# Performance work log

Hardware: AMD Instinct MI355X
Metric: run time of the kernel (lower is better)

The kernel has to match this reference:

```python
import jax, jax.numpy as jnp
import numpy as np


def _gather_corner(flat_feats, iz, iy, ix, H, W, B, F, Hg, Wg):
    # flat_feats: [B, F, D*H*W]; iz/iy/ix: [B, Hg, Wg] int32 (already clamped)
    lin = (iz * H + iy) * W + ix                      # [B, Hg, Wg]
    lin = jnp.broadcast_to(lin.reshape(B, 1, Hg * Wg), (B, F, Hg * Wg))
    return jnp.take_along_axis(flat_feats, lin, axis=2).reshape(B, F, Hg, Wg)


def setup_inputs() -> dict:
    key = jax.random.key(0)
    k1, k2 = jax.random.split(key)
    input_feats = jax.random.normal(k1, (4, 8, 128, 128, 128), dtype=jnp.float32)
    sampling_grid = jax.random.normal(k2, (4, 512, 512, 3), dtype=jnp.float32)
    return {"input_feats": input_feats, "sampling_grid": sampling_grid}


def reference(input_feats, sampling_grid):
    B, F, D, H, W = input_feats.shape
    Hg, Wg = sampling_grid.shape[1], sampling_grid.shape[2]

    # map grid from [-1,1] to voxel coordinates [0, dim-1]
    g = jnp.clip(sampling_grid, -1.0, 1.0)
    scale = jnp.array([W - 1.0, H - 1.0, D - 1.0], dtype=sampling_grid.dtype)
    g = (g + 1.0) * 0.5 * scale                      # [B, Hg, Wg, 3] in x,y,z order
    x, y, z = g[..., 0], g[..., 1], g[..., 2]

    x0 = jnp.floor(x); y0 = jnp.floor(y); z0 = jnp.floor(z)
    u = (x - x0)[:, None]                            # [B,1,Hg,Wg]
    v = (y - y0)[:, None]
    w = (z - z0)[:, None]

    # nearest grid_sample with align_corners=True on integer coords == clamped index
    def clampi(a, hi):
        return jnp.clip(a, 0, hi).astype(jnp.int32)

    ix0 = clampi(x0, W - 1); ix1 = clampi(x0 + 1.0, W - 1)
    iy0 = clampi(y0, H - 1); iy1 = clampi(y0 + 1.0, H - 1)
    iz0 = clampi(z0, D - 1); iz1 = clampi(z0 + 1.0, D - 1)

    flat = input_feats.reshape(B, F, D * H * W)
    gc = lambda iz, iy, ix: _gather_corner(flat, iz, iy, ix, H, W, B, F, Hg, Wg)

    c000 = gc(iz0, iy0, ix0); c001 = gc(iz1, iy0, ix0)
    c010 = gc(iz0, iy1, ix0); c011 = gc(iz1, iy1, ix0)
    c100 = gc(iz0, iy0, ix1); c101 = gc(iz1, iy0, ix1)
    c110 = gc(iz0, iy1, ix1); c111 = gc(iz1, iy1, ix1)

    out = ((1 - u) * (1 - v) * (1 - w) * c000 + (1 - u) * (1 - v) * w * c001
           + (1 - u) * v * (1 - w) * c010 + (1 - u) * v * w * c011
           + u * (1 - v) * (1 - w) * c100 + u * (1 - v) * w * c101
           + u * v * (1 - w) * c110 + u * v * w * c111)
    return out  # [B, F, Hg, Wg]
```

## Files before the change

kernel.cpp:

```cpp
#include <hip/hip_runtime.h>
#include <hip/hip_fp16.h>


#define NB 4
#define NF 8
#define ND 128
#define NH 128
#define NW 128
#define HG 512
#define WG 512

__global__ __launch_bounds__(256) void transform_kernel(
    const float* __restrict__ feats, __half* __restrict__ T)
{
    const size_t S = (size_t)ND * NH * NW;
    size_t tid = (size_t)blockIdx.x * blockDim.x + threadIdx.x;
    size_t b  = tid / (S / 4);
    size_t s4 = (tid - b * (S / 4)) * 4;

    const float* fb = feats + b * NF * S;
    __half* tb = T + (b * S + s4) * NF;

    float4 vals[NF];
#pragma unroll
    for (int f = 0; f < NF; ++f)
        vals[f] = *(const float4*)(fb + (size_t)f * S + s4);

#pragma unroll
    for (int i = 0; i < 4; ++i) {
        alignas(16) __half2 hv[4];
#pragma unroll
        for (int f = 0; f < 4; ++f) {
            float a = ((const float*)&vals[2 * f])[i];
            float c = ((const float*)&vals[2 * f + 1])[i];
            hv[f] = __floats2half2_rn(a, c);
        }
        *(uint4*)(tb + (size_t)i * NF) = *(const uint4*)hv;
    }
}

__device__ __forceinline__ void row_accum(
    const __half* __restrict__ tb, size_t rowbase, bool hi,
    float wr, float um, float u, float acc[NF])
{
    uint4 lov = *(const uint4*)(tb + rowbase);
    uint4 hiv = *(const uint4*)(tb + rowbase + NF);
    uint4 c0 = hi ? hiv : lov;
    const uint4& c1 = hiv;

    const unsigned* p0 = (const unsigned*)&c0;
    const unsigned* p1 = (const unsigned*)&c1;
#pragma unroll
    for (int j = 0; j < 4; ++j) {
        unsigned u0 = p0[j], u1 = p1[j];
        float2 f0 = __half22float2(*(const __half2*)&u0);
        float2 f1 = __half22float2(*(const __half2*)&u1);
        acc[2 * j]     += wr * (um * f0.x + u * f1.x);
        acc[2 * j + 1] += wr * (um * f0.y + u * f1.y);
    }
}

__global__ __launch_bounds__(256) void trilerp_half_kernel(
    const __half* __restrict__ T,
    const float* __restrict__ grid,
    float* __restrict__ out)
{
    const int P = HG * WG;
    int idx = blockIdx.x * blockDim.x + threadIdx.x;
    int b = idx >> 18;
    int p = idx & (P - 1);

    const float* g = grid + (size_t)idx * 3;
    float x = g[0], y = g[1], z = g[2];

    x = fminf(fmaxf(x, -1.0f), 1.0f);
    y = fminf(fmaxf(y, -1.0f), 1.0f);
    z = fminf(fmaxf(z, -1.0f), 1.0f);
    x = (x + 1.0f) * 0.5f * (float)(NW - 1);
    y = (y + 1.0f) * 0.5f * (float)(NH - 1);
    z = (z + 1.0f) * 0.5f * (float)(ND - 1);

    float xf = floorf(x), yf = floorf(y), zf = floorf(z);
    float u = x - xf, v = y - yf, w = z - zf;
    float um = 1.0f - u, vm = 1.0f - v, wm = 1.0f - w;

    int ix0 = min(max((int)xf, 0), NW - 1);
    int iy0 = min(max((int)yf, 0), NH - 1);
    int iy1 = min(iy0 + 1, NH - 1);
    int iz0 = min(max((int)zf, 0), ND - 1);
    int iz1 = min(iz0 + 1, ND - 1);

    int xb = min(ix0, NW - 2);
    bool hi = (ix0 != xb);

    const __half* tb = T + (size_t)b * ((size_t)ND * NH * NW) * NF;
    size_t r00 = ((size_t)(iz0 * NH + iy0) * NW + xb) * NF;
    size_t r01 = ((size_t)(iz0 * NH + iy1) * NW + xb) * NF;
    size_t r10 = ((size_t)(iz1 * NH + iy0) * NW + xb) * NF;
    size_t r11 = ((size_t)(iz1 * NH + iy1) * NW + xb) * NF;

    float acc[NF];
#pragma unroll
    for (int f = 0; f < NF; ++f) acc[f] = 0.0f;

    row_accum(tb, r00, hi, wm * vm, um, u, acc);
    row_accum(tb, r01, hi, wm * v,  um, u, acc);
    row_accum(tb, r10, hi, w  * vm, um, u, acc);
    row_accum(tb, r11, hi, w  * v,  um, u, acc);

    float* o = out + (size_t)b * NF * P + p;
#pragma unroll
    for (int f = 0; f < NF; ++f)
        o[(size_t)f * P] = acc[f];
}

__global__ __launch_bounds__(256) void trilerp_f32_kernel(
    const float* __restrict__ feats,
    const float* __restrict__ grid,
    float* __restrict__ out)
{
    const int P = HG * WG;
    int idx = blockIdx.x * blockDim.x + threadIdx.x;
    int b = idx >> 18;
    int p = idx & (P - 1);

    const float* g = grid + (size_t)idx * 3;
    float x = g[0], y = g[1], z = g[2];
    x = fminf(fmaxf(x, -1.0f), 1.0f);
    y = fminf(fmaxf(y, -1.0f), 1.0f);
    z = fminf(fmaxf(z, -1.0f), 1.0f);
    x = (x + 1.0f) * 0.5f * (float)(NW - 1);
    y = (y + 1.0f) * 0.5f * (float)(NH - 1);
    z = (z + 1.0f) * 0.5f * (float)(ND - 1);

    float xf = floorf(x), yf = floorf(y), zf = floorf(z);
    float u = x - xf, v = y - yf, w = z - zf;

    int ix0 = min(max((int)xf, 0), NW - 1);
    int ix1 = min(ix0 + 1, NW - 1);
    int iy0 = min(max((int)yf, 0), NH - 1);
    int iy1 = min(iy0 + 1, NH - 1);
    int iz0 = min(max((int)zf, 0), ND - 1);
    int iz1 = min(iz0 + 1, ND - 1);

    float um = 1.0f - u, vm = 1.0f - v, wm = 1.0f - w;
    float w000 = um * vm * wm, w100 = u * vm * wm;
    float w010 = um * v * wm,  w110 = u * v * wm;
    float w001 = um * vm * w,  w101 = u * vm * w;
    float w011 = um * v * w,   w111 = u * v * w;

    int off00 = (iz0 * NH + iy0) * NW;
    int off01 = (iz0 * NH + iy1) * NW;
    int off10 = (iz1 * NH + iy0) * NW;
    int off11 = (iz1 * NH + iy1) * NW;

    const size_t fstride = (size_t)ND * NH * NW;
    const float* fb = feats + (size_t)b * NF * fstride;
    float* o = out + (size_t)b * NF * P + p;

#pragma unroll
    for (int f = 0; f < NF; ++f) {
        const float* fp = fb + (size_t)f * fstride;
        float r = w000 * fp[off00 + ix0] + w100 * fp[off00 + ix1]
                + w010 * fp[off01 + ix0] + w110 * fp[off01 + ix1]
                + w001 * fp[off10 + ix0] + w101 * fp[off10 + ix1]
                + w011 * fp[off11 + ix0] + w111 * fp[off11 + ix1];
        o[(size_t)f * P] = r;
    }
}

extern "C" void kernel_launch(void* const* d_in, const int* in_sizes, int n_in,
                              void* d_out, int out_size, void* d_ws, size_t ws_size,
                              hipStream_t stream) {
    const float* feats = (const float*)d_in[0];
    const float* grid  = (const float*)d_in[1];
    float* out = (float*)d_out;

    const size_t needed = (size_t)NB * ND * NH * NW * NF * sizeof(__half);

    if (ws_size >= needed) {
        __half* T = (__half*)d_ws;
        const int tthreads = NB * ND * NH * NW / 4;
        transform_kernel<<<tthreads / 256, 256, 0, stream>>>(feats, T);
        const int total = NB * HG * WG;
        trilerp_half_kernel<<<total / 256, 256, 0, stream>>>(T, grid, out);
    } else {
        const int total = NB * HG * WG;
        trilerp_f32_kernel<<<total / 256, 256, 0, stream>>>(feats, grid, out);
    }
}
```

Before: 446.2 us.

## Pipeline per-batch fp16 transform with gather of previous batch in one launch

Replaces the two full-size launches with a sequence of per-batch stage launches. Each launch splits its blocks between converting batch k to the fp16 channel-interleaved layout and gathering/interpolating batch k-1, so the bandwidth-bound transform overlaps with the latency-bound gather. It adds extra launches and grid-stride loops, and each half gets only 1024 blocks, which may leave one phase underutilized or imbalanced.

```diff
diff --git a/kernel.cpp b/kernel.cpp
--- a/kernel.cpp
+++ b/kernel.cpp
@@ -10,32 +10,36 @@
 #define HG 512
 #define WG 512
 
-__global__ __launch_bounds__(256) void transform_kernel(
-    const float* __restrict__ feats, __half* __restrict__ T)
-{
-    const size_t S = (size_t)ND * NH * NW;
-    size_t tid = (size_t)blockIdx.x * blockDim.x + threadIdx.x;
-    size_t b  = tid / (S / 4);
-    size_t s4 = (tid - b * (S / 4)) * 4;
-
-    const float* fb = feats + b * NF * S;
-    __half* tb = T + (b * S + s4) * NF;
-
-    float4 vals[NF];
-#pragma unroll
-    for (int f = 0; f < NF; ++f)
-        vals[f] = *(const float4*)(fb + (size_t)f * S + s4);
-
-#pragma unroll
-    for (int i = 0; i < 4; ++i) {
-        alignas(16) __half2 hv[4];
-#pragma unroll
-        for (int f = 0; f < 4; ++f) {
-            float a = ((const float*)&vals[2 * f])[i];
-            float c = ((const float*)&vals[2 * f + 1])[i];
-            hv[f] = __floats2half2_rn(a, c);
+#define SVOX ((size_t)ND * NH * NW)
+#define NPTS (HG * WG)
+
+__device__ __forceinline__ void do_transform(
+    const float* __restrict__ feats, __half* __restrict__ T,
+    int b, int tid, int nthreads)
+{
+    const float* fb = feats + (size_t)b * NF * SVOX;
+    const int nitems = (int)(SVOX / 4);
+
+    for (int it = tid; it < nitems; it += nthreads) {
+        size_t s4 = (size_t)it * 4;
+        __half* tb = T + ((size_t)b * SVOX + s4) * NF;
+
+        float4 vals[NF];
+#pragma unroll
+        for (int f = 0; f < NF; ++f)
+            vals[f] = *(const float4*)(fb + (size_t)f * SVOX + s4);
+
+#pragma unroll
+        for (int i = 0; i < 4; ++i) {
+            alignas(16) __half2 hv[4];
+#pragma unroll
+            for (int f = 0; f < 4; ++f) {
+                float a = ((const float*)&vals[2 * f])[i];
+                float c = ((const float*)&vals[2 * f + 1])[i];
+                hv[f] = __floats2half2_rn(a, c);
+            }
+            *(uint4*)(tb + (size_t)i * NF) = *(const uint4*)hv;
         }
-        *(uint4*)(tb + (size_t)i * NF) = *(const uint4*)hv;
     }
 }
 
@@ -60,58 +64,72 @@
     }
 }
 
-__global__ __launch_bounds__(256) void trilerp_half_kernel(
-    const __half* __restrict__ T,
-    const float* __restrict__ grid,
-    float* __restrict__ out)
-{
-    const int P = HG * WG;
-    int idx = blockIdx.x * blockDim.x + threadIdx.x;
-    int b = idx >> 18;
-    int p = idx & (P - 1);
-
-    const float* g = grid + (size_t)idx * 3;
-    float x = g[0], y = g[1], z = g[2];
-
-    x = fminf(fmaxf(x, -1.0f), 1.0f);
-    y = fminf(fmaxf(y, -1.0f), 1.0f);
-    z = fminf(fmaxf(z, -1.0f), 1.0f);
-    x = (x + 1.0f) * 0.5f * (float)(NW - 1);
-    y = (y + 1.0f) * 0.5f * (float)(NH - 1);
-    z = (z + 1.0f) * 0.5f * (float)(ND - 1);
-
-    float xf = floorf(x), yf = floorf(y), zf = floorf(z);
-    float u = x - xf, v = y - yf, w = z - zf;
-    float um = 1.0f - u, vm = 1.0f - v, wm = 1.0f - w;
-
-    int ix0 = min(max((int)xf, 0), NW - 1);
-    int iy0 = min(max((int)yf, 0), NH - 1);
-    int iy1 = min(iy0 + 1, NH - 1);
-    int iz0 = min(max((int)zf, 0), ND - 1);
-    int iz1 = min(iz0 + 1, ND - 1);
-
-    int xb = min(ix0, NW - 2);
-    bool hi = (ix0 != xb);
-
-    const __half* tb = T + (size_t)b * ((size_t)ND * NH * NW) * NF;
-    size_t r00 = ((size_t)(iz0 * NH + iy0) * NW + xb) * NF;
-    size_t r01 = ((size_t)(iz0 * NH + iy1) * NW + xb) * NF;
-    size_t r10 = ((size_t)(iz1 * NH + iy0) * NW + xb) * NF;
-    size_t r11 = ((size_t)(iz1 * NH + iy1) * NW + xb) * NF;
-
-    float acc[NF];
-#pragma unroll
-    for (int f = 0; f < NF; ++f) acc[f] = 0.0f;
-
-    row_accum(tb, r00, hi, wm * vm, um, u, acc);
-    row_accum(tb, r01, hi, wm * v,  um, u, acc);
-    row_accum(tb, r10, hi, w  * vm, um, u, acc);
-    row_accum(tb, r11, hi, w  * v,  um, u, acc);
-
-    float* o = out + (size_t)b * NF * P + p;
-#pragma unroll
-    for (int f = 0; f < NF; ++f)
-        o[(size_t)f * P] = acc[f];
+__device__ __forceinline__ void do_gather(
+    const __half* __restrict__ T, const float* __restrict__ grid,
+    float* __restrict__ out, int b, int tid, int nthreads)
+{
+    for (int p = tid; p < NPTS; p += nthreads) {
+        const float* g = grid + ((size_t)b * NPTS + p) * 3;
+        float x = g[0], y = g[1], z = g[2];
+
+        x = fminf(fmaxf(x, -1.0f), 1.0f);
+        y = fminf(fmaxf(y, -1.0f), 1.0f);
+        z = fminf(fmaxf(z, -1.0f), 1.0f);
+        x = (x + 1.0f) * 0.5f * (float)(NW - 1);
+        y = (y + 1.0f) * 0.5f * (float)(NH - 1);
+        z = (z + 1.0f) * 0.5f * (float)(ND - 1);
+
+        float xf = floorf(x), yf = floorf(y), zf = floorf(z);
+        float u = x - xf, v = y - yf, w = z - zf;
+        float um = 1.0f - u, vm = 1.0f - v, wm = 1.0f - w;
+
+        int ix0 = min(max((int)xf, 0), NW - 1);
+        int iy0 = min(max((int)yf, 0), NH - 1);
+        int iy1 = min(iy0 + 1, NH - 1);
+        int iz0 = min(max((int)zf, 0), ND - 1);
+        int iz1 = min(iz0 + 1, ND - 1);
+
+        int xb = min(ix0, NW - 2);
+        bool hi = (ix0 != xb);
+
+        const __half* tb = T + (size_t)b * SVOX * NF;
+        size_t r00 = ((size_t)(iz0 * NH + iy0) * NW + xb) * NF;
+        size_t r01 = ((size_t)(iz0 * NH + iy1) * NW + xb) * NF;
+        size_t r10 = ((size_t)(iz1 * NH + iy0) * NW + xb) * NF;
+        size_t r11 = ((size_t)(iz1 * NH + iy1) * NW + xb) * NF;
+
+        float acc[NF];
+#pragma unroll
+        for (int f = 0; f < NF; ++f) acc[f] = 0.0f;
+
+        row_accum(tb, r00, hi, wm * vm, um, u, acc);
+        row_accum(tb, r01, hi, wm * v,  um, u, acc);
+        row_accum(tb, r10, hi, w  * vm, um, u, acc);
+        row_accum(tb, r11, hi, w  * v,  um, u, acc);
+
+        float* o = out + (size_t)b * NF * NPTS + p;
+#pragma unroll
+        for (int f = 0; f < NF; ++f)
+            o[(size_t)f * NPTS] = acc[f];
+    }
+}
+
+__global__ __launch_bounds__(256) void stage_kernel(
+    const float* __restrict__ feats, const float* __restrict__ grid,
+    float* __restrict__ out, __half* __restrict__ T,
+    int tb, int gb, int splitA)
+{
+    int blk = blockIdx.x;
+    if (blk < splitA) {
+        if (tb >= 0)
+            do_transform(feats, T, tb, blk * 256 + (int)threadIdx.x, splitA * 256);
+    } else {
+        if (gb >= 0) {
+            int nB = (int)gridDim.x - splitA;
+            do_gather(T, grid, out, gb, (blk - splitA) * 256 + (int)threadIdx.x,
+                      nB * 256);
+        }
+    }
 }
 
 __global__ __launch_bounds__(256) void trilerp_f32_kernel(
@@ -119,7 +137,7 @@
     const float* __restrict__ grid,
     float* __restrict__ out)
 {
-    const int P = HG * WG;
+    const int P = NPTS;
     int idx = blockIdx.x * blockDim.x + threadIdx.x;
     int b = idx >> 18;
     int p = idx & (P - 1);
@@ -154,13 +172,12 @@
     int off10 = (iz1 * NH + iy0) * NW;
     int off11 = (iz1 * NH + iy1) * NW;
 
-    const size_t fstride = (size_t)ND * NH * NW;
-    const float* fb = feats + (size_t)b * NF * fstride;
+    const float* fb = feats + (size_t)b * NF * SVOX;
     float* o = out + (size_t)b * NF * P + p;
 
 #pragma unroll
     for (int f = 0; f < NF; ++f) {
-        const float* fp = fb + (size_t)f * fstride;
+        const float* fp = fb + (size_t)f * SVOX;
         float r = w000 * fp[off00 + ix0] + w100 * fp[off00 + ix1]
                 + w010 * fp[off01 + ix0] + w110 * fp[off01 + ix1]
                 + w001 * fp[off10 + ix0] + w101 * fp[off10 + ix1]
@@ -176,14 +193,17 @@
     const float* grid  = (const float*)d_in[1];
     float* out = (float*)d_out;
 
-    const size_t needed = (size_t)NB * ND * NH * NW * NF * sizeof(__half);
+    const size_t needed = (size_t)NB * SVOX * NF * sizeof(__half);
 
     if (ws_size >= needed) {
         __half* T = (__half*)d_ws;
-        const int tthreads = NB * ND * NH * NW / 4;
-        transform_kernel<<<tthreads / 256, 256, 0, stream>>>(feats, T);
-        const int total = NB * HG * WG;
-        trilerp_half_kernel<<<total / 256, 256, 0, stream>>>(T, grid, out);
+        const int NBLK = 2048;
+        dim3 block(256);
+        stage_kernel<<<NBLK, block, 0, stream>>>(feats, grid, out, T, 0, -1, NBLK);
+        for (int k = 1; k < NB; ++k)
+            stage_kernel<<<NBLK, block, 0, stream>>>(feats, grid, out, T, k, k - 1,
+                                                     NBLK / 2);
+        stage_kernel<<<NBLK, block, 0, stream>>>(feats, grid, out, T, -1, NB - 1, 0);
     } else {
         const int total = NB * HG * WG;
         trilerp_f32_kernel<<<total / 256, 256, 0, stream>>>(feats, grid, out);
```

Result: no change. 448.3 us (+0.5%).
